# Kernel optimization log

Hardware: AMD Instinct MI355X
Metric: run time of the kernel (lower is better)

## Reference

```python
import jax, jax.numpy as jnp
import numpy as np

B, C, H, W = 2, 64, 128, 128
KH = KW = 3
K = KH * KW
PAD = 1


def conv(x, w, b, pad):
    out = jax.lax.conv_general_dilated(
        x, w, window_strides=(1, 1), padding=[(pad, pad), (pad, pad)],
        dimension_numbers=("NCHW", "OIHW", "NCHW"))
    return out + b[None, :, None, None]


def leaky_relu(x, slope=0.2):
    return jnp.where(x >= 0, x, slope * x)


def deform_conv(img, offset, mask, w, b):
    # img: [B,C,Hi,Wi]; offset: [B,2K,H,W] (dy,dx interleaved per tap); mask: [B,K,H,W]
    Bb, Ci, Hi, Wi = img.shape
    Ho, Wo = offset.shape[2], offset.shape[3]
    off = offset.reshape(Bb, K, 2, Ho, Wo)
    dy, dx = off[:, :, 0], off[:, :, 1]
    ki, kj = jnp.meshgrid(jnp.arange(KH), jnp.arange(KW), indexing="ij")
    ki = ki.reshape(K).astype(img.dtype)
    kj = kj.reshape(K).astype(img.dtype)
    base_h = (jnp.arange(Ho) - PAD).astype(img.dtype)
    base_w = (jnp.arange(Wo) - PAD).astype(img.dtype)
    ys = base_h[None, None, :, None] + ki[None, :, None, None] + dy  # [B,K,Ho,Wo]
    xs = base_w[None, None, None, :] + kj[None, :, None, None] + dx

    y0 = jnp.floor(ys)
    x0 = jnp.floor(xs)
    ty = ys - y0
    tx = xs - x0
    y0i = y0.astype(jnp.int32)
    x0i = x0.astype(jnp.int32)
    flat = img.reshape(Bb, Ci, Hi * Wi)

    def corner(yi, xi, wgt):
        valid = (yi >= 0) & (yi < Hi) & (xi >= 0) & (xi < Wi)
        yc = jnp.clip(yi, 0, Hi - 1)
        xc = jnp.clip(xi, 0, Wi - 1)
        idx = (yc * Wi + xc).reshape(Bb, 1, -1)
        v = jnp.take_along_axis(flat, jnp.broadcast_to(idx, (Bb, Ci, idx.shape[-1])), axis=2)
        v = v.reshape(Bb, Ci, K, Ho, Wo)
        return v * (wgt * valid.astype(img.dtype))[:, None]

    samp = (corner(y0i, x0i, (1 - ty) * (1 - tx))
            + corner(y0i, x0i + 1, (1 - ty) * tx)
            + corner(y0i + 1, x0i, ty * (1 - tx))
            + corner(y0i + 1, x0i + 1, ty * tx))  # [B,C,K,Ho,Wo]
    out = jnp.einsum("ock,bckhw->bohw", w.reshape(w.shape[0], Ci, K), samp * mask[:, None])
    return out + b[None, :, None, None]


def setup_inputs() -> dict:
    key = jax.random.key(0)
    ks = jax.random.split(key, 8)
    s = 0.05  # keep predicted offsets in a realistic few-pixel range
    return {
        "x": jax.random.normal(ks[0], (B, C, H, W), jnp.float32),
        "y": jax.random.normal(ks[1], (B, C, H, W), jnp.float32),
        "w0": jax.random.normal(ks[2], (C, C, 1, 1), jnp.float32) * s,
        "b0": jnp.zeros((C,), jnp.float32),
        "w_om": jax.random.normal(ks[3], (3 * K, 2 * C, KH, KW), jnp.float32) * s,
        "b_om": jnp.zeros((3 * K,), jnp.float32),
        "w_dc": jax.random.normal(ks[4], (C, C, KH, KW), jnp.float32) * s,
        "b_dc": jnp.zeros((C,), jnp.float32),
        "w1": jax.random.normal(ks[5], (C, C, KH, KW), jnp.float32) * s,
        "b1": jnp.zeros((C,), jnp.float32),
        "w2": jax.random.normal(ks[6], (C, C, KH, KW), jnp.float32) * s,
        "b2": jnp.zeros((C,), jnp.float32),
    }


def reference(x, y, w0, b0, w_om, b_om, w_dc, b_dc, w1, b1, w2, b2):
    x0 = conv(x, w0, b0, pad=0)  # 1x1 projection
    om = conv(jnp.concatenate([x0, y], axis=1), w_om, b_om, pad=PAD)
    offset = om[:, : 2 * K]
    mask = 2.0 * jax.nn.sigmoid(om[:, 2 * K :])
    out = x0 + deform_conv(y, offset, mask, w_dc, b_dc)
    return conv(leaky_relu(conv(out, w1, b1, pad=PAD)), w2, b2, pad=PAD) + out
```

## Files before the change

### kernel.cpp

```cpp
#include <hip/hip_runtime.h>
#include <hip/hip_bf16.h>
#include <math.h>

#define BB 2
#define CCH 64
#define HH 128
#define WWD 128
#define HWv (HH*WWD)
#define KK 9
#define KSTEP 18
#define OMKS 36
#define RCOLS 66
#define CSTR 72
#define CSTR2 136
#define DROW 584

typedef __attribute__((ext_vector_type(8))) short bf16x8;
typedef __attribute__((ext_vector_type(4))) float f32x4;
typedef unsigned short u16;
typedef unsigned int u32;

__device__ inline u16 f2bf(float f) {
  __hip_bfloat16 h = __float2bfloat16(f);
  return *reinterpret_cast<u16*>(&h);
}
__device__ inline u32 f2bf2(float lo, float hi) {
  return ((u32)f2bf(hi) << 16) | (u32)f2bf(lo);
}
__device__ inline float bfLO(u32 v) { return __uint_as_float(v << 16); }
__device__ inline float bfHI(u32 v) { return __uint_as_float(v & 0xffff0000u); }
__device__ inline float bf2f(u16 v) { return __uint_as_float((u32)v << 16); }

__global__ __launch_bounds__(256) void pack_all_k(
    const float* __restrict__ w_dc, const float* __restrict__ w1,
    const float* __restrict__ w2, const float* __restrict__ w_om,
    const float* __restrict__ w0, u16* __restrict__ pk_dc,
    u16* __restrict__ pk_w1, u16* __restrict__ pk_w2,
    u16* __restrict__ pk_om, u16* __restrict__ pk_0) {
  int blk = blockIdx.x;
  int tid = threadIdx.x;
  if (blk < 432) {
    const float* w = blk < 144 ? w_dc : (blk < 288 ? w1 : w2);
    u16* dst = blk < 144 ? pk_dc : (blk < 288 ? pk_w1 : pk_w2);
    int idx = (blk % 144) * 256 + tid;
    int j = idx & 7, l = (idx >> 3) & 63;
    int s = (idx >> 9) % 18, q = idx / 9216;
    int co = q * 16 + (l & 15);
    int kp = s * 32 + (l >> 4) * 8 + j;
    dst[idx] = f2bf(w[(co * 64 + (kp & 63)) * 9 + (kp >> 6)]);
  } else if (blk < 576) {
    int idx = (blk - 432) * 256 + tid;
    int j = idx & 7, l = (idx >> 3) & 63;
    int s = (idx >> 9) % 36, q = idx / 18432;
    int co = q * 16 + (l & 15);
    int kp = s * 32 + (l >> 4) * 8 + j;
    pk_om[idx] = (co < 27)
        ? f2bf(w_om[(co * 128 + (kp & 127)) * 9 + (kp >> 7)]) : (u16)0;
  } else {
    int idx = (blk - 576) * 256 + tid;
    int j = idx & 7, l = (idx >> 3) & 63;
    int s = (idx >> 9) & 1, q = idx / 1024;
    int co = q * 16 + (l & 15);
    int k = s * 32 + (l >> 4) * 8 + j;
    pk_0[idx] = f2bf(w0[co * 64 + k]);
  }
}

__global__ __launch_bounds__(256) void conv1x1y_k(const float* __restrict__ x,
    const float* __restrict__ y, const u16* __restrict__ wpack,
    const float* __restrict__ b0, u16* __restrict__ x0bf,
    u16* __restrict__ yt) {
  #define S1ROW 72
  __shared__ __align__(16) float smem[64 * 65];
  u16* samp1 = (u16*)smem;
  int tid = threadIdx.x;
  int lane = tid & 63, q = tid >> 6;
  int pixbase = blockIdx.x * 64;
  int hwb = pixbase & (HWv - 1);
  int b = pixbase >> 14;

  {
    const float* src = y + (size_t)b * CCH * HWv;
    #pragma unroll
    for (int i = 0; i < 16; i++) {
      int ci = i * 4 + q;
      smem[ci * 65 + lane] = src[(size_t)ci * HWv + hwb + lane];
    }
    __syncthreads();
    u32* dst32 = (u32*)(yt + ((size_t)b * HWv + hwb) * 64);
    int lane2 = tid & 31, rr = tid >> 5;
    #pragma unroll
    for (int i = 0; i < 8; i++) {
      int row = i * 8 + rr;
      dst32[row * 32 + lane2] = f2bf2(smem[(2 * lane2) * 65 + row],
                                      smem[(2 * lane2 + 1) * 65 + row]);
    }
    __syncthreads();
  }

  {
    u16 tmp[16];
    #pragma unroll
    for (int i = 0; i < 16; i++) {
      int ci = q * 16 + i;
      tmp[i] = f2bf(x[((size_t)b * CCH + ci) * HWv + hwb + lane]);
    }
    #pragma unroll
    for (int i = 0; i < 2; i++)
      *(bf16x8*)(samp1 + lane * S1ROW + q * 16 + i * 8) = *(bf16x8*)(tmp + i * 8);
  }
  __syncthreads();
  f32x4 acc[4] = {{0,0,0,0},{0,0,0,0},{0,0,0,0},{0,0,0,0}};
  int g = lane >> 4;
  const bf16x8* bp = (const bf16x8*)wpack + (size_t)(q * 2) * 64 + lane;
  #pragma unroll
  for (int s = 0; s < 2; s++) {
    bf16x8 bf = bp[(size_t)s * 64];
    #pragma unroll
    for (int t = 0; t < 4; t++) {
      bf16x8 a = *(const bf16x8*)(samp1 + (t * 16 + (lane & 15)) * S1ROW + g * 8 + s * 32);
      acc[t] = __builtin_amdgcn_mfma_f32_16x16x32_bf16(a, bf, acc[t], 0, 0, 0);
    }
  }
  int co = q * 16 + (lane & 15);
  float bv = b0[co];
  u16* dst = x0bf + ((size_t)b * HWv + hwb + g * 4) * 64 + co;
  #pragma unroll
  for (int t = 0; t < 4; t++)
    #pragma unroll
    for (int r = 0; r < 4; r++)
      dst[(size_t)(t * 16 + r) * 64] = f2bf(acc[t][r] + bv);
}

__global__ __launch_bounds__(512) void omd_k(const u16* __restrict__ x0bf,
    const u16* __restrict__ yt, const u16* __restrict__ pk_om,
    const u16* __restrict__ pk_dc, const float* __restrict__ b_om,
    const float* __restrict__ b_dc, u16* __restrict__ ob) {
  __shared__ __align__(16) u16 A[3 * RCOLS * CSTR2];
  __shared__ __align__(16) float omv[64 * 28];
  u32* A32 = (u32*)A;
  u32* dsamp32 = (u32*)A;
  u16* dsamp = A;
  int (*prm)[8] = (int(*)[8])(A + 18688);
  int tid = threadIdx.x;
  int lane = tid & 63, q = tid >> 6;
  int pixbase = blockIdx.x * 64;
  int hwb = pixbase & (HWv - 1);
  int b = pixbase >> 14;
  int h = hwb >> 7, wb = hwb & 127;
  const u32* x0b32 = (const u32*)x0bf + (size_t)b * HWv * 32;
  const u32* yt32  = (const u32*)yt + (size_t)b * HWv * 32;

  {
    int lane2 = tid & 31, hw16 = tid >> 5;
    int cofs = lane2 * 2;
    const u32* srcb = (lane2 < 16) ? (x0b32 + cofs) : (yt32 + cofs - 32);
    #pragma unroll
    for (int i = 0; i < 13; i++) {
      int u = hw16 + 16 * i;
      if (u < 198) {
        int r = u / 66, c = u % 66;
        int hh = h - 1 + r, ww = wb - 1 + c;
        uint2 v = {0u, 0u};
        if ((unsigned)hh < HH && (unsigned)ww < WWD)
          v = *(const uint2*)(srcb + (size_t)(hh * WWD + ww) * 32);
        *(uint2*)(A32 + u * (CSTR2 / 2) + cofs) = v;
      }
    }
  }
  __syncthreads();

  {
    int cohalf = q & 1, pxg = q >> 1;
    f32x4 acc = {0.f, 0.f, 0.f, 0.f};
    const bf16x8* bp = (const bf16x8*)pk_om + (size_t)(cohalf * OMKS) * 64 + lane;
    #pragma unroll
    for (int s = 0; s < OMKS; s++) {
      int kk = s >> 2;
      int addr = ((kk / 3) * 66 + pxg * 16 + (lane & 15) + (kk % 3)) * CSTR2
                 + (s & 3) * 32 + (lane >> 4) * 8;
      bf16x8 a = *(const bf16x8*)(A + addr);
      acc = __builtin_amdgcn_mfma_f32_16x16x32_bf16(a, bp[(size_t)s * 64], acc, 0, 0, 0);
    }
    int co = cohalf * 16 + (lane & 15);
    if (co < 27) {
      float bv = b_om[co];
      int px = pxg * 16 + (lane >> 4) * 4;
      #pragma unroll
      for (int r = 0; r < 4; r++)
        omv[(px + r) * 28 + co] = acc[r] + bv;
    }
  }
  __syncthreads();

  for (int h2 = 0; h2 < 2; h2++) {
    if (tid < 32 * KK) {
      int pl = tid / KK, k = tid % KK;
      const float* omp = omv + (h2 * 32 + pl) * 28;
      float dy = omp[2 * k], dx = omp[2 * k + 1];
      float mk = 2.f / (1.f + expf(-omp[18 + k]));
      float ys = (float)(h - 1 + k / 3) + dy;
      float xs = (float)(wb + h2 * 32 + pl - 1 + k % 3) + dx;
      float y0f = floorf(ys), x0f = floorf(xs);
      float ty = ys - y0f, tx = xs - x0f;
      int yi = (int)y0f, xi = (int)x0f;
      bool y0v = (unsigned)yi < HH, y1v = (unsigned)(yi + 1) < HH;
      bool x0v = (unsigned)xi < WWD, x1v = (unsigned)(xi + 1) < WWD;
      float w00 = (1.f - ty) * (1.f - tx) * mk * ((y0v && x0v) ? 1.f : 0.f);
      float w01 = (1.f - ty) * tx * mk * ((y0v && x1v) ? 1.f : 0.f);
      float w10 = ty * (1.f - tx) * mk * ((y1v && x0v) ? 1.f : 0.f);
      float w11 = ty * tx * mk * ((y1v && x1v) ? 1.f : 0.f);
      int* p = prm[tid];
      *(int4*)p = make_int4(min(max(yi, 0), HH - 1) * (WWD * 32),
                            min(max(yi + 1, 0), HH - 1) * (WWD * 32),
                            min(max(xi, 0), WWD - 1) * 32,
                            min(max(xi + 1, 0), WWD - 1) * 32);
      *(int4*)(p + 4) = make_int4(__float_as_int(w00), __float_as_int(w01),
                                  __float_as_int(w10), __float_as_int(w11));
    }
    __syncthreads();
    {
      int lane4 = tid & 15, g16 = tid >> 4;
      const u32* ytb = yt32 + lane4 * 2;
      #pragma unroll
      for (int i = 0; i < 9; i++) {
        int u = g16 + 32 * i;
        int k = u % 9, pix = u / 9;
        int4 pa = *(const int4*)prm[u];
        int4 pb = *(const int4*)(prm[u] + 4);
        uint2 v00 = *(const uint2*)(ytb + pa.x + pa.z);
        uint2 v01 = *(const uint2*)(ytb + pa.x + pa.w);
        uint2 v10 = *(const uint2*)(ytb + pa.y + pa.z);
        uint2 v11 = *(const uint2*)(ytb + pa.y + pa.w);
        float w00 = __int_as_float(pb.x), w01 = __int_as_float(pb.y);
        float w10 = __int_as_float(pb.z), w11 = __int_as_float(pb.w);
        float a0 = fmaf(bfLO(v00.x), w00, fmaf(bfLO(v01.x), w01,
                   fmaf(bfLO(v10.x), w10, bfLO(v11.x) * w11)));
        float a1 = fmaf(bfHI(v00.x), w00, fmaf(bfHI(v01.x), w01,
                   fmaf(bfHI(v10.x), w10, bfHI(v11.x) * w11)));
        float a2 = fmaf(bfLO(v00.y), w00, fmaf(bfLO(v01.y), w01,
                   fmaf(bfLO(v10.y), w10, bfLO(v11.y) * w11)));
        float a3 = fmaf(bfHI(v00.y), w00, fmaf(bfHI(v01.y), w01,
                   fmaf(bfHI(v10.y), w10, bfHI(v11.y) * w11)));
        uint2 o = {f2bf2(a0, a1), f2bf2(a2, a3)};
        *(uint2*)(dsamp32 + pix * (DROW / 2) + k * 32 + lane4 * 2) = o;
      }
    }
    __syncthreads();
    {
      int qq = q & 3, pxg = q >> 2;
      f32x4 acc = {0.f, 0.f, 0.f, 0.f};
      const u16* arow = dsamp + (pxg * 16 + (lane & 15)) * DROW + (lane >> 4) * 8;
      const bf16x8* bp = (const bf16x8*)pk_dc + (size_t)(qq * KSTEP) * 64 + lane;
      #pragma unroll
      for (int s = 0; s < KSTEP; s++) {
        bf16x8 a = *(const bf16x8*)(arow + s * 32);
        acc = __builtin_amdgcn_mfma_f32_16x16x32_bf16(a, bp[(size_t)s * 64], acc, 0, 0, 0);
      }
      int co = qq * 16 + (lane & 15);
      int px = h2 * 32 + pxg * 16 + (lane >> 4) * 4;
      float bv = b_dc[co];
      size_t obase = ((size_t)b * HWv + hwb + px) * 64 + co;
      #pragma unroll
      for (int r = 0; r < 4; r++)
        ob[obase + (size_t)r * 64] =
            f2bf(acc[r] + bv + bf2f(x0bf[obase + (size_t)r * 64]));
    }
    __syncthreads();
  }
}

template <int MODE>
__global__ __launch_bounds__(512) void rconv_k(const u16* __restrict__ in,
    const u16* __restrict__ res, const u16* __restrict__ wpack,
    const float* __restrict__ bias, void* __restrict__ outp) {
  __shared__ __align__(16) u16 samp[3 * RCOLS * CSTR];
  u32* samp32 = (u32*)samp;
  int tid = threadIdx.x;
  int pixbase = blockIdx.x * 64;
  int hwb = pixbase & (HWv - 1);
  int b = pixbase >> 14;
  int h = hwb >> 7, wb = hwb & 127;

  {
    int lane4 = tid & 15, g16 = tid >> 4;
    const u32* inb = (const u32*)in + (size_t)b * HWv * 32 + lane4 * 2;
    #pragma unroll
    for (int i = 0; i < 7; i++) {
      int u = g16 + 32 * i;
      if (u < 198) {
        int r = u / 66, c = u % 66;
        int hh = h - 1 + r, ww = wb - 1 + c;
        uint2 v = {0u, 0u};
        if ((unsigned)hh < HH && (unsigned)ww < WWD)
          v = *(const uint2*)(inb + (size_t)(hh * WWD + ww) * 32);
        *(uint2*)(samp32 + (r * 66 + c) * (CSTR / 2) + lane4 * 2) = v;
      }
    }
  }
  __syncthreads();

  int lane = tid & 63, q = tid >> 6;
  int copair = q & 1, pxg = q >> 1;
  f32x4 acc[2] = {{0,0,0,0},{0,0,0,0}};
  const bf16x8* bp = (const bf16x8*)wpack + (size_t)(copair * 2 * KSTEP) * 64 + lane;
  #pragma unroll
  for (int s = 0; s < KSTEP; s++) {
    int kk = s >> 1;
    int addr = ((kk / 3) * 66 + pxg * 16 + (lane & 15) + (kk % 3)) * CSTR
               + (s & 1) * 32 + (lane >> 4) * 8;
    bf16x8 a = *(const bf16x8*)(samp + addr);
    acc[0] = __builtin_amdgcn_mfma_f32_16x16x32_bf16(a, bp[(size_t)s * 64], acc[0], 0, 0, 0);
    acc[1] = __builtin_amdgcn_mfma_f32_16x16x32_bf16(a, bp[(size_t)(KSTEP + s) * 64], acc[1], 0, 0, 0);
  }

  int px = pxg * 16 + (lane >> 4) * 4;
  if (MODE == 1) {
    u16* outb = (u16*)outp;
    #pragma unroll
    for (int t = 0; t < 2; t++) {
      int co = copair * 32 + t * 16 + (lane & 15);
      float bv = bias[co];
      size_t obase = ((size_t)b * HWv + hwb + px) * 64 + co;
      #pragma unroll
      for (int r = 0; r < 4; r++) {
        float v = acc[t][r] + bv;
        outb[obase + (size_t)r * 64] = f2bf(v >= 0.f ? v : 0.2f * v);
      }
    }
  } else {
    float* outf = (float*)outp;
    float* ot = (float*)samp;
    __syncthreads();
    #pragma unroll
    for (int t = 0; t < 2; t++) {
      int co = copair * 32 + t * 16 + (lane & 15);
      float bv = bias[co];
      size_t rbase = ((size_t)b * HWv + hwb + px) * 64 + co;
      #pragma unroll
      for (int r = 0; r < 4; r++)
        ot[co * 68 + px + r] = acc[t][r] + bv + bf2f(res[rbase + (size_t)r * 64]);
    }
    __syncthreads();
    int co = tid >> 3, seg = tid & 7;
    const float4* src4 = (const float4*)(ot + co * 68 + seg * 8);
    float4 v0 = src4[0], v1 = src4[1];
    float* dst = outf + ((size_t)b * CCH + co) * HWv + hwb + seg * 8;
    *(float4*)dst = v0;
    *(float4*)(dst + 4) = v1;
  }
}

extern "C" void kernel_launch(void* const* d_in, const int* in_sizes, int n_in,
                              void* d_out, int out_size, void* d_ws, size_t ws_size,
                              hipStream_t stream) {
  const float* x    = (const float*)d_in[0];
  const float* y    = (const float*)d_in[1];
  const float* w0   = (const float*)d_in[2];
  const float* b0   = (const float*)d_in[3];
  const float* w_om = (const float*)d_in[4];
  const float* b_om = (const float*)d_in[5];
  const float* w_dc = (const float*)d_in[6];
  const float* b_dc = (const float*)d_in[7];
  const float* w1   = (const float*)d_in[8];
  const float* b1   = (const float*)d_in[9];
  const float* w2   = (const float*)d_in[10];
  const float* b2   = (const float*)d_in[11];
  float* out = (float*)d_out;

  const size_t NFULL = (size_t)BB * CCH * HWv;
  const size_t NPACK = 4 * KSTEP * 64 * 8;
  const size_t NPACKOM = 2 * OMKS * 64 * 8;
  u16* x0bf = (u16*)d_ws;
  u16* ob   = x0bf + NFULL;
  u16* z1   = ob + NFULL;
  u16* yt   = z1;
  u16* pk_dc = z1 + NFULL;
  u16* pk_w1 = pk_dc + NPACK;
  u16* pk_w2 = pk_w1 + NPACK;
  u16* pk_om = pk_w2 + NPACK;
  u16* pk_0  = pk_om + NPACKOM;

  pack_all_k<<<592, 256, 0, stream>>>(w_dc, w1, w2, w_om, w0,
                                      pk_dc, pk_w1, pk_w2, pk_om, pk_0);
  conv1x1y_k<<<(int)((size_t)BB * HWv / 64), 256, 0, stream>>>(
      x, y, pk_0, b0, x0bf, yt);
  omd_k<<<(int)((size_t)BB * HWv / 64), 512, 0, stream>>>(
      x0bf, yt, pk_om, pk_dc, b_om, b_dc, ob);
  rconv_k<1><<<(int)((size_t)BB * HWv / 64), 512, 0, stream>>>(ob, nullptr, pk_w1, b1, z1);
  rconv_k<2><<<(int)((size_t)BB * HWv / 64), 512, 0, stream>>>(z1, ob, pk_w2, b2, out);
}
```

Before: 65.22 us.

## Retile 3x3 conv kernels from 1x64 strips to 2x32 pixel tiles

Changes the per-block output tile in the offset/deform kernel and both residual conv kernels from one row of 64 pixels to two rows of 32 pixels. The staged halo shrinks from 3x66 to 4x34 positions, so each block loads fewer halo pixels from global memory and uses less LDS. Wave-to-pixel mappings, output addressing and the transposed fp32 store in the final kernel are rewritten to match. The deform stage now handles one output row per h2 iteration. Global stores become shorter contiguous runs, and the deform sampling parameter buffer moves to its own shared array, which adds LDS.

```diff
diff --git a/kernel.cpp b/kernel.cpp
--- a/kernel.cpp
+++ b/kernel.cpp
@@ -10,7 +10,7 @@
 #define KK 9
 #define KSTEP 18
 #define OMKS 36
-#define RCOLS 66
+#define TCOLS 34
 #define CSTR 72
 #define CSTR2 136
 #define DROW 584
@@ -136,31 +136,30 @@
     const u16* __restrict__ yt, const u16* __restrict__ pk_om,
     const u16* __restrict__ pk_dc, const float* __restrict__ b_om,
     const float* __restrict__ b_dc, u16* __restrict__ ob) {
-  __shared__ __align__(16) u16 A[3 * RCOLS * CSTR2];
+  __shared__ __align__(16) u16 A[18688];
+  __shared__ __align__(16) int prm[288][8];
   __shared__ __align__(16) float omv[64 * 28];
   u32* A32 = (u32*)A;
   u32* dsamp32 = (u32*)A;
   u16* dsamp = A;
-  int (*prm)[8] = (int(*)[8])(A + 18688);
   int tid = threadIdx.x;
   int lane = tid & 63, q = tid >> 6;
-  int pixbase = blockIdx.x * 64;
-  int hwb = pixbase & (HWv - 1);
-  int b = pixbase >> 14;
-  int h = hwb >> 7, wb = hwb & 127;
+  int blk = blockIdx.x;
+  int wq = blk & 3, rp = (blk >> 2) & 63, b = blk >> 8;
+  int h0 = rp * 2, wb = wq * 32;
   const u32* x0b32 = (const u32*)x0bf + (size_t)b * HWv * 32;
   const u32* yt32  = (const u32*)yt + (size_t)b * HWv * 32;
 
   {
-    int lane2 = tid & 31, hw16 = tid >> 5;
+    int lane2 = tid & 31, g16 = tid >> 5;
     int cofs = lane2 * 2;
     const u32* srcb = (lane2 < 16) ? (x0b32 + cofs) : (yt32 + cofs - 32);
     #pragma unroll
-    for (int i = 0; i < 13; i++) {
-      int u = hw16 + 16 * i;
-      if (u < 198) {
-        int r = u / 66, c = u % 66;
-        int hh = h - 1 + r, ww = wb - 1 + c;
+    for (int i = 0; i < 9; i++) {
+      int u = g16 + 16 * i;
+      if (u < 4 * TCOLS) {
+        int r = u / TCOLS, c = u % TCOLS;
+        int hh = h0 - 1 + r, ww = wb - 1 + c;
         uint2 v = {0u, 0u};
         if ((unsigned)hh < HH && (unsigned)ww < WWD)
           v = *(const uint2*)(srcb + (size_t)(hh * WWD + ww) * 32);
@@ -171,13 +170,13 @@
   __syncthreads();
 
   {
-    int cohalf = q & 1, pxg = q >> 1;
+    int r = q & 1, cg = (q >> 1) & 1, cohalf = q >> 2;
     f32x4 acc = {0.f, 0.f, 0.f, 0.f};
     const bf16x8* bp = (const bf16x8*)pk_om + (size_t)(cohalf * OMKS) * 64 + lane;
     #pragma unroll
     for (int s = 0; s < OMKS; s++) {
       int kk = s >> 2;
-      int addr = ((kk / 3) * 66 + pxg * 16 + (lane & 15) + (kk % 3)) * CSTR2
+      int addr = ((r + kk / 3) * TCOLS + cg * 16 + (lane & 15) + (kk % 3)) * CSTR2
                  + (s & 3) * 32 + (lane >> 4) * 8;
       bf16x8 a = *(const bf16x8*)(A + addr);
       acc = __builtin_amdgcn_mfma_f32_16x16x32_bf16(a, bp[(size_t)s * 64], acc, 0, 0, 0);
@@ -185,10 +184,10 @@
     int co = cohalf * 16 + (lane & 15);
     if (co < 27) {
       float bv = b_om[co];
-      int px = pxg * 16 + (lane >> 4) * 4;
-      #pragma unroll
-      for (int r = 0; r < 4; r++)
-        omv[(px + r) * 28 + co] = acc[r] + bv;
+      int px = r * 32 + cg * 16 + (lane >> 4) * 4;
+      #pragma unroll
+      for (int j = 0; j < 4; j++)
+        omv[(px + j) * 28 + co] = acc[j] + bv;
     }
   }
   __syncthreads();
@@ -199,8 +198,8 @@
       const float* omp = omv + (h2 * 32 + pl) * 28;
       float dy = omp[2 * k], dx = omp[2 * k + 1];
       float mk = 2.f / (1.f + expf(-omp[18 + k]));
-      float ys = (float)(h - 1 + k / 3) + dy;
-      float xs = (float)(wb + h2 * 32 + pl - 1 + k % 3) + dx;
+      float ys = (float)(h0 + h2 - 1 + k / 3) + dy;
+      float xs = (float)(wb + pl - 1 + k % 3) + dx;
       float y0f = floorf(ys), x0f = floorf(xs);
       float ty = ys - y0f, tx = xs - x0f;
       int yi = (int)y0f, xi = (int)x0f;
@@ -258,13 +257,13 @@
         acc = __builtin_amdgcn_mfma_f32_16x16x32_bf16(a, bp[(size_t)s * 64], acc, 0, 0, 0);
       }
       int co = qq * 16 + (lane & 15);
-      int px = h2 * 32 + pxg * 16 + (lane >> 4) * 4;
+      int px = pxg * 16 + (lane >> 4) * 4;
       float bv = b_dc[co];
-      size_t obase = ((size_t)b * HWv + hwb + px) * 64 + co;
-      #pragma unroll
-      for (int r = 0; r < 4; r++)
-        ob[obase + (size_t)r * 64] =
-            f2bf(acc[r] + bv + bf2f(x0bf[obase + (size_t)r * 64]));
+      size_t obase = ((size_t)b * HWv + (h0 + h2) * WWD + wb + px) * 64 + co;
+      #pragma unroll
+      for (int j = 0; j < 4; j++)
+        ob[obase + (size_t)j * 64] =
+            f2bf(acc[j] + bv + bf2f(x0bf[obase + (size_t)j * 64]));
     }
     __syncthreads();
   }
@@ -274,58 +273,58 @@
 __global__ __launch_bounds__(512) void rconv_k(const u16* __restrict__ in,
     const u16* __restrict__ res, const u16* __restrict__ wpack,
     const float* __restrict__ bias, void* __restrict__ outp) {
-  __shared__ __align__(16) u16 samp[3 * RCOLS * CSTR];
+  __shared__ __align__(16) u16 samp[4 * TCOLS * CSTR];
   u32* samp32 = (u32*)samp;
   int tid = threadIdx.x;
-  int pixbase = blockIdx.x * 64;
-  int hwb = pixbase & (HWv - 1);
-  int b = pixbase >> 14;
-  int h = hwb >> 7, wb = hwb & 127;
+  int blk = blockIdx.x;
+  int wq = blk & 3, rp = (blk >> 2) & 63, b = blk >> 8;
+  int h0 = rp * 2, wb = wq * 32;
 
   {
     int lane4 = tid & 15, g16 = tid >> 4;
     const u32* inb = (const u32*)in + (size_t)b * HWv * 32 + lane4 * 2;
     #pragma unroll
-    for (int i = 0; i < 7; i++) {
+    for (int i = 0; i < 5; i++) {
       int u = g16 + 32 * i;
-      if (u < 198) {
-        int r = u / 66, c = u % 66;
-        int hh = h - 1 + r, ww = wb - 1 + c;
+      if (u < 4 * TCOLS) {
+        int r = u / TCOLS, c = u % TCOLS;
+        int hh = h0 - 1 + r, ww = wb - 1 + c;
         uint2 v = {0u, 0u};
         if ((unsigned)hh < HH && (unsigned)ww < WWD)
           v = *(const uint2*)(inb + (size_t)(hh * WWD + ww) * 32);
-        *(uint2*)(samp32 + (r * 66 + c) * (CSTR / 2) + lane4 * 2) = v;
+        *(uint2*)(samp32 + u * (CSTR / 2) + lane4 * 2) = v;
       }
     }
   }
   __syncthreads();
 
   int lane = tid & 63, q = tid >> 6;
-  int copair = q & 1, pxg = q >> 1;
+  int r = q & 1, cg = (q >> 1) & 1, copair = q >> 2;
   f32x4 acc[2] = {{0,0,0,0},{0,0,0,0}};
   const bf16x8* bp = (const bf16x8*)wpack + (size_t)(copair * 2 * KSTEP) * 64 + lane;
   #pragma unroll
   for (int s = 0; s < KSTEP; s++) {
     int kk = s >> 1;
-    int addr = ((kk / 3) * 66 + pxg * 16 + (lane & 15) + (kk % 3)) * CSTR
+    int addr = ((r + kk / 3) * TCOLS + cg * 16 + (lane & 15) + (kk % 3)) * CSTR
                + (s & 1) * 32 + (lane >> 4) * 8;
     bf16x8 a = *(const bf16x8*)(samp + addr);
     acc[0] = __builtin_amdgcn_mfma_f32_16x16x32_bf16(a, bp[(size_t)s * 64], acc[0], 0, 0, 0);
     acc[1] = __builtin_amdgcn_mfma_f32_16x16x32_bf16(a, bp[(size_t)(KSTEP + s) * 64], acc[1], 0, 0, 0);
   }
 
-  int px = pxg * 16 + (lane >> 4) * 4;
+  int pxc = cg * 16 + (lane >> 4) * 4;
+  int hwp = (h0 + r) * WWD + wb + pxc;
   if (MODE == 1) {
     u16* outb = (u16*)outp;
     #pragma unroll
     for (int t = 0; t < 2; t++) {
       int co = copair * 32 + t * 16 + (lane & 15);
       float bv = bias[co];
-      size_t obase = ((size_t)b * HWv + hwb + px) * 64 + co;
-      #pragma unroll
-      for (int r = 0; r < 4; r++) {
-        float v = acc[t][r] + bv;
-        outb[obase + (size_t)r * 64] = f2bf(v >= 0.f ? v : 0.2f * v);
+      size_t obase = ((size_t)b * HWv + hwp) * 64 + co;
+      #pragma unroll
+      for (int j = 0; j < 4; j++) {
+        float v = acc[t][j] + bv;
+        outb[obase + (size_t)j * 64] = f2bf(v >= 0.f ? v : 0.2f * v);
       }
     }
   } else {
@@ -336,16 +335,17 @@
     for (int t = 0; t < 2; t++) {
       int co = copair * 32 + t * 16 + (lane & 15);
       float bv = bias[co];
-      size_t rbase = ((size_t)b * HWv + hwb + px) * 64 + co;
-      #pragma unroll
-      for (int r = 0; r < 4; r++)
-        ot[co * 68 + px + r] = acc[t][r] + bv + bf2f(res[rbase + (size_t)r * 64]);
+      size_t rbase = ((size_t)b * HWv + hwp) * 64 + co;
+      #pragma unroll
+      for (int j = 0; j < 4; j++)
+        ot[co * 72 + r * 36 + pxc + j] = acc[t][j] + bv + bf2f(res[rbase + (size_t)j * 64]);
     }
     __syncthreads();
     int co = tid >> 3, seg = tid & 7;
-    const float4* src4 = (const float4*)(ot + co * 68 + seg * 8);
+    int r2 = seg >> 2, c8 = (seg & 3) * 8;
+    const float4* src4 = (const float4*)(ot + co * 72 + r2 * 36 + c8);
     float4 v0 = src4[0], v1 = src4[1];
-    float* dst = outf + ((size_t)b * CCH + co) * HWv + hwb + seg * 8;
+    float* dst = outf + ((size_t)b * CCH + co) * HWv + (h0 + r2) * WWD + wb + c8;
     *(float4*)dst = v0;
     *(float4*)(dst + 4) = v1;
   }
@@ -381,12 +381,12 @@
   u16* pk_om = pk_w2 + NPACK;
   u16* pk_0  = pk_om + NPACKOM;
 
+  const int NB = (int)((size_t)BB * HWv / 64);
+
   pack_all_k<<<592, 256, 0, stream>>>(w_dc, w1, w2, w_om, w0,
                                       pk_dc, pk_w1, pk_w2, pk_om, pk_0);
-  conv1x1y_k<<<(int)((size_t)BB * HWv / 64), 256, 0, stream>>>(
-      x, y, pk_0, b0, x0bf, yt);
-  omd_k<<<(int)((size_t)BB * HWv / 64), 512, 0, stream>>>(
-      x0bf, yt, pk_om, pk_dc, b_om, b_dc, ob);
-  rconv_k<1><<<(int)((size_t)BB * HWv / 64), 512, 0, stream>>>(ob, nullptr, pk_w1, b1, z1);
-  rconv_k<2><<<(int)((size_t)BB * HWv / 64), 512, 0, stream>>>(z1, ob, pk_w2, b2, out);
-}
+  conv1x1y_k<<<NB, 256, 0, stream>>>(x, y, pk_0, b0, x0bf, yt);
+  omd_k<<<NB, 512, 0, stream>>>(x0bf, yt, pk_om, pk_dc, b_om, b_dc, ob);
+  rconv_k<1><<<NB, 512, 0, stream>>>(ob, nullptr, pk_w1, b1, z1);
+  rconv_k<2><<<NB, 512, 0, stream>>>(z1, ob, pk_w2, b2, out);
+}
```

Result: faster. 63.86 us (median of 2 runs) (-2.1%).
